# Performance work log

Measured on AMD Instinct MI355X. Metric: run time of the kernel, lower is better.

## Reference

```python
import jax, jax.numpy as jnp
import numpy as np

SR = 16000
N_FFT = 400
HOP = 160
N_MELS = 128
F_MIN = 0.0
F_MAX = 8000.0
PCEN_ALPHA = 0.8
PCEN_SMOOTH = 0.04
PCEN_DELTA = 2.0
PCEN_ROOT = 2.0
PCEN_FLOOR = 1e-08
TARGET = (192, 128)


def _hz_to_mel(f):
    return 2595.0 * np.log10(1.0 + f / 700.0)


def _mel_to_hz(m):
    return 700.0 * (10.0 ** (m / 2595.0) - 1.0)


def _mel_filterbank():
    # torchaudio melscale_fbanks, mel_scale='htk', norm=None
    n_freqs = N_FFT // 2 + 1  # 201
    all_freqs = np.linspace(0.0, SR / 2, n_freqs)
    m_pts = np.linspace(_hz_to_mel(F_MIN), _hz_to_mel(F_MAX), N_MELS + 2)
    f_pts = _mel_to_hz(m_pts)
    f_diff = f_pts[1:] - f_pts[:-1]  # (n_mels+1,)
    slopes = f_pts[None, :] - all_freqs[:, None]  # (n_freqs, n_mels+2)
    down = -slopes[:, :-2] / f_diff[:-1]
    up = slopes[:, 2:] / f_diff[1:]
    fb = np.maximum(0.0, np.minimum(down, up))  # (n_freqs, n_mels)
    return jnp.asarray(fb, dtype=jnp.float32)


def _hann_window():
    # periodic hann, matches torch.hann_window(400)
    n = np.arange(N_FFT)
    return jnp.asarray(0.5 * (1.0 - np.cos(2.0 * np.pi * n / N_FFT)), dtype=jnp.float32)


def setup_inputs() -> dict:
    key = jax.random.key(0)
    audio = jax.random.normal(key, (2048, 32000), dtype=jnp.float32)
    return {"audio": audio}


def _mel_spectrogram(audio):
    # center=True reflect pad by n_fft//2
    pad = N_FFT // 2
    x = jnp.pad(audio, ((0, 0), (pad, pad)), mode='reflect')  # (N, 32400)
    T = (x.shape[1] - N_FFT) // HOP + 1  # 201
    idx = jnp.arange(T)[:, None] * HOP + jnp.arange(N_FFT)[None, :]  # (T, n_fft)
    frames = x[:, idx] * _hann_window()  # (N, T, n_fft)
    spec = jnp.fft.rfft(frames, axis=-1)  # (N, T, 201)
    power = jnp.abs(spec) ** 2
    mel = jnp.einsum('ntf,fm->ntm', power, _mel_filterbank())  # (N, T, n_mels)
    return mel


def _pcen(mel_ntm):
    # IIR smoothing over time via scan; mel_ntm: (N, T, M)
    s = PCEN_SMOOTH
    mel_t = jnp.transpose(mel_ntm, (1, 0, 2))  # (T, N, M)

    def step(m_prev, e):
        m_new = (1.0 - s) * m_prev + s * e
        return m_new, m_new

    m0 = mel_t[0]
    _, Ms = jax.lax.scan(step, m0, mel_t[1:])
    M = jnp.concatenate([m0[None], Ms], axis=0)  # (T, N, Mels)
    M = jnp.transpose(M, (1, 0, 2))  # (N, T, Mels)
    inv_r = 1.0 / PCEN_ROOT
    return (mel_ntm / (PCEN_FLOOR + M) ** PCEN_ALPHA + PCEN_DELTA) ** inv_r - PCEN_DELTA ** inv_r


def reference(audio):
    mel = _mel_spectrogram(audio)          # (N, T, 128); original is (N,128,T), PCEN over time either way
    pcen = _pcen(mel)                      # (N, T, 128) == original after transpose(1,2)
    x = pcen[:, None, :, :]                # (N, 1, T, 128)
    N = x.shape[0]
    # bilinear, align_corners=False == jax.image 'linear' (half-pixel centers)
    out = jax.image.resize(x, (N, 1, TARGET[0], TARGET[1]), method='linear')
    return out
```

## Files before the change

kernel.cpp:

```cpp
#include <hip/hip_runtime.h>
#include <math.h>

typedef __attribute__((ext_vector_type(8))) _Float16 half8;
typedef __attribute__((ext_vector_type(4))) float f32x4;
typedef __attribute__((ext_vector_type(4))) unsigned int u32x4;

namespace {
constexpr int NS = 32000, PAD = 200, NT = 201, TOUT = 192, NMEL = 128;
constexpr int FRB = 48, NSTRIP = 5;
constexpr int AU_SPAN = 7936;
constexpr int PW_STRIDE = 232, PW_ROWS = 48;
constexpr int BAS_NT = 28;
constexpr int BAS_ELEMS = 13 * 28 * 64 * 8;
constexpr int FB_ELEMS  = 7 * 8 * 64 * 8;
constexpr int OUT_ROW_U16 = TOUT * NMEL * 2;
constexpr int MEL_OFF_U16 = OUT_ROW_U16 - NT * NMEL;
}

__device__ __forceinline__ int swz(int e) { return e ^ (((e >> 7) & 3) << 3); }
__device__ __forceinline__ unsigned short f2h(float f) {
  _Float16 h = (_Float16)f; return __builtin_bit_cast(unsigned short, h);
}
__device__ __forceinline__ float h2f(unsigned short u) {
  return (float)__builtin_bit_cast(_Float16, u);
}

__global__ void setup_tables(unsigned short* __restrict__ ws) {
  int idx = blockIdx.x * 256 + threadIdx.x;
  if (idx < BAS_ELEMS) {
    int j = idx & 7, lane = (idx >> 3) & 63, rest = idx >> 9;
    int nt = rest % BAS_NT, ks = rest / BAS_NT;
    int k   = ks * 32 + ((lane >> 4) << 3) + j;
    int col = nt * 16 + (lane & 15);
    float v = 0.f;
    if (k < 400 && col < 402) {
      int bin = col >> 1;
      int mm  = (k * bin) % 400;
      float th = (float)mm * 0.015707963267948967f;
      float tr = (col & 1) ? sinf(th) : cosf(th);
      float wn = 0.5f * (1.0f - cosf((float)k * 0.015707963267948967f));
      v = wn * tr;
    }
    ws[idx] = f2h(v);
  } else if (idx < BAS_ELEMS + FB_ELEMS) {
    int i2 = idx - BAS_ELEMS;
    int j = i2 & 7, lane = (i2 >> 3) & 63, rest = i2 >> 9;
    int nt = rest % 8, ks = rest / 8;
    int k   = ks * 32 + ((lane >> 4) << 3) + j;
    int mel = nt * 16 + (lane & 15);
    float v = 0.f;
    if (k <= 200) {
      double mhi = 2595.0 * log10(1.0 + 8000.0 / 700.0);
      double ml = mhi * (double)mel / 129.0;
      double mc = mhi * (double)(mel + 1) / 129.0;
      double mr = mhi * (double)(mel + 2) / 129.0;
      double fl = 700.0 * (pow(10.0, ml / 2595.0) - 1.0);
      double fc = 700.0 * (pow(10.0, mc / 2595.0) - 1.0);
      double fr = 700.0 * (pow(10.0, mr / 2595.0) - 1.0);
      double f  = 40.0 * (double)k;
      double wv = fmin((f - fl) / (fc - fl), (fr - f) / (fr - fc));
      v = (float)fmax(0.0, wv);
    }
    ws[idx] = f2h(v);
  }
}

__global__ __launch_bounds__(256) __attribute__((amdgpu_waves_per_eu(4)))
void dft_mel_kernel(const float* __restrict__ audio, const unsigned short* __restrict__ ws,
                    unsigned short* __restrict__ outu)
{
  __shared__ unsigned short au[AU_SPAN];
  __shared__ unsigned short pw16[PW_ROWS * PW_STRIDE];
  const int tid = threadIdx.x;
  const int bid = blockIdx.x;
  const int r = bid / NSTRIP, s = bid % NSTRIP;
  const int t0 = s * FRB;
  const float* __restrict__ ab = audio + (size_t)r * NS;
  const int g0 = t0 * 160 - PAD;

  {
    const int nchunk = AU_SPAN / 8;
    const int live   = (s == NSTRIP - 1) ? 224 : nchunk;
    #pragma unroll 4
    for (int ci = tid; ci < nchunk; ci += 256) {
      half8 hv;
      if (ci >= live) {
        hv = (half8){0, 0, 0, 0, 0, 0, 0, 0};
      } else {
        int gbase = g0 + ci * 8;
        if (gbase >= 0 && gbase + 7 < NS) {
          const float4* p = (const float4*)(ab + gbase);
          float4 x0 = p[0], x1 = p[1];
          hv[0] = (_Float16)x0.x; hv[1] = (_Float16)x0.y;
          hv[2] = (_Float16)x0.z; hv[3] = (_Float16)x0.w;
          hv[4] = (_Float16)x1.x; hv[5] = (_Float16)x1.y;
          hv[6] = (_Float16)x1.z; hv[7] = (_Float16)x1.w;
        } else {
          #pragma unroll
          for (int j = 0; j < 8; ++j) {
            int g = gbase + j;
            if (g < 0) g = -g;
            if (g >= NS) g = 2 * NS - 2 - g;
            hv[j] = (_Float16)ab[g];
          }
        }
      }
      *(half8*)(au + swz(ci * 8)) = hv;
    }
  }
  for (int i = tid; i < PW_ROWS * 32; i += 256) {
    int row = i >> 5, sl = i & 31;
    if (sl) pw16[row * PW_STRIDE + 200 + sl] = 0;
  }
  __syncthreads();

  const int w = tid >> 6, lane = tid & 63, lr = lane & 15, lg = lane >> 4;

  f32x4 acc[3][7];
  #pragma unroll
  for (int mm = 0; mm < 3; ++mm)
    #pragma unroll
    for (int n = 0; n < 7; ++n) acc[mm][n] = (f32x4){0.f, 0.f, 0.f, 0.f};
  {
    const int laneA = lr * 160 + lg * 8;
    for (int ks = 0; ks < 13; ++ks) {
      half8 Af[3];
      #pragma unroll
      for (int mm = 0; mm < 3; ++mm)
        Af[mm] = *(const half8*)(au + swz(mm * 2560 + ks * 32 + laneA));
      const unsigned short* bsrc = ws + ((size_t)((ks * BAS_NT + w * 7) * 64 + lane)) * 8;
      #pragma unroll
      for (int n = 0; n < 7; ++n) {
        half8 Bf = *(const half8*)(bsrc + n * 512);
        #pragma unroll
        for (int mm = 0; mm < 3; ++mm)
          acc[mm][n] = __builtin_amdgcn_mfma_f32_16x16x32_f16(Af[mm], Bf, acc[mm][n], 0, 0, 0);
      }
    }
  }

  #pragma unroll
  for (int mm = 0; mm < 3; ++mm) {
    #pragma unroll
    for (int n = 0; n < 7; ++n) {
      int gcol = (w * 7 + n) * 16 + lr;
      #pragma unroll
      for (int j = 0; j < 4; ++j) {
        float v = acc[mm][n][j];
        float q = __shfl_xor(v, 1);
        int row = mm * 16 + lg * 4 + j;
        if (!(gcol & 1) && gcol < 402)
          pw16[row * PW_STRIDE + (gcol >> 1)] = f2h(fmaf(v, v, q * q));
      }
    }
  }
  __syncthreads();

  #pragma unroll
  for (int mt = 0; mt < 3; ++mt) {
    #pragma unroll
    for (int nt = 0; nt < 2; ++nt) {
      f32x4 a2 = (f32x4){0.f, 0.f, 0.f, 0.f};
      const unsigned short* psrc = pw16 + (mt * 16 + lr) * PW_STRIDE + lg * 8;
      const unsigned short* fsrc = ws + BAS_ELEMS + ((size_t)(2 * w + nt) * 64 + lane) * 8;
      #pragma unroll
      for (int ks = 0; ks < 7; ++ks)
        a2 = __builtin_amdgcn_mfma_f32_16x16x32_f16(*(const half8*)(psrc + ks * 32),
                                                    *(const half8*)(fsrc + (size_t)ks * 4096),
                                                    a2, 0, 0, 0);
      int gm = (2 * w + nt) * 16 + lr;
      #pragma unroll
      for (int j = 0; j < 4; ++j) {
        int t = t0 + mt * 16 + lg * 4 + j;
        if (t < NT)
          outu[(size_t)r * OUT_ROW_U16 + MEL_OFF_U16 + t * NMEL + gm] = f2h(a2[j]);
      }
    }
  }
}

__global__ __launch_bounds__(512)
void pcen_resize_kernel(unsigned short* __restrict__ outu)
{
  __shared__ unsigned short mel[NT * NMEL];
  __shared__ float carry[4][NMEL];
  __shared__ float minb[4][NMEL];
  const int tid = threadIdx.x;
  const int r = blockIdx.x;
  const unsigned short* src = outu + (size_t)r * OUT_ROW_U16 + MEL_OFF_U16;
  for (int i = tid; i < (NT * NMEL) / 8; i += 512)
    *(u32x4*)(mel + i * 8) = *(const u32x4*)(src + (size_t)i * 8);
  __syncthreads();

  const int m = tid & 127, c = tid >> 7;
  const int t0  = (c == 0) ? 0 : (51 + 50 * (c - 1));
  const int len = (c == 0) ? 51 : 50;

  float M = 0.f;
  for (int t = t0; t < t0 + len; ++t) {
    float e = h2f(mel[t * NMEL + m]);
    M = (t == 0) ? e : fmaf(0.96f, M, 0.04f * e);
  }
  carry[c][m] = M;
  __syncthreads();
  if (c == 0) {
    float a50 = exp2f(50.0f * log2f(0.96f));
    float m1 = carry[0][m];
    float m2 = fmaf(a50, m1, carry[1][m]);
    float m3 = fmaf(a50, m2, carry[2][m]);
    minb[1][m] = m1; minb[2][m] = m2; minb[3][m] = m3;
  }
  __syncthreads();

  float Min = (c == 0) ? 0.f : minb[c][m];
  float wf = 1.f, Mloc = 0.f;
  for (int t = t0; t < t0 + len; ++t) {
    float e = h2f(mel[t * NMEL + m]);
    Mloc = (t == 0) ? e : fmaf(0.96f, Mloc, 0.04f * e);
    wf *= 0.96f;
    float Mt = fmaf(wf, Min, Mloc);
    float dn = exp2f(0.8f * log2f(1e-8f + Mt));
    float pc = sqrtf(e / dn + 2.0f) - 1.41421356237309515f;
    mel[t * NMEL + m] = f2h(pc);
  }
  __syncthreads();

  float* __restrict__ ob = (float*)outu + (size_t)r * TOUT * NMEL;
  const float INVS = 201.0f / 192.0f;
  for (int i = c; i < TOUT; i += 4) {
    float ct = ((float)i + 0.5f) * INVS - 0.5f;
    int jlo = (int)ceilf(ct - INVS);
    int jhi = (int)floorf(ct + INVS);
    if (jlo < 0) jlo = 0;
    if (jhi > NT - 1) jhi = NT - 1;
    float wsum = 0.f, val = 0.f;
    for (int j = jlo; j <= jhi; ++j) {
      float wv = 1.0f - fabsf((float)j - ct) / INVS;
      if (wv > 0.f) { wsum += wv; val = fmaf(wv, h2f(mel[j * NMEL + m]), val); }
    }
    ob[(size_t)i * NMEL + m] = val / wsum;
  }
}

extern "C" void kernel_launch(void* const* d_in, const int* in_sizes, int n_in,
                              void* d_out, int out_size, void* d_ws, size_t ws_size,
                              hipStream_t stream) {
  (void)in_sizes; (void)n_in; (void)out_size; (void)ws_size;
  unsigned short* ws = (unsigned short*)d_ws;
  setup_tables<<<(BAS_ELEMS + FB_ELEMS + 255) / 256, 256, 0, stream>>>(ws);
  dft_mel_kernel<<<2048 * NSTRIP, 256, 0, stream>>>((const float*)d_in[0], ws,
                                                    (unsigned short*)d_out);
  pcen_resize_kernel<<<2048, 512, 0, stream>>>((unsigned short*)d_out);
}
```

Before: 458.9 us.

## Split DFT-mel into full strips plus small tail kernel, prefetch basis

The old strip decomposition ran five 48-frame strips per row, and the last strip mostly computed zero-padded frames. The kernel is now templated: four full 48-frame strips per row, plus a separate single-tile launch for the remaining frames 192-200, so less padding work is done. The DFT loop now software-prefetches the next basis fragment. The shuffle is replaced by a DPP swap, and each lane writes its power values without a parity-conditional store. The filterbank fragments are hoisted into registers and reused across row tiles, and waves_per_eu is lowered to 3. An extra kernel launch and higher register pressure may offset some of this.

New measurement: 464.7 us. About the same (+1.3%).

```diff
diff --git a/kernel.cpp b/kernel.cpp
--- a/kernel.cpp
+++ b/kernel.cpp
@@ -7,9 +7,7 @@
 
 namespace {
 constexpr int NS = 32000, PAD = 200, NT = 201, TOUT = 192, NMEL = 128;
-constexpr int FRB = 48, NSTRIP = 5;
-constexpr int AU_SPAN = 7936;
-constexpr int PW_STRIDE = 232, PW_ROWS = 48;
+constexpr int PW_STRIDE = 236;
 constexpr int BAS_NT = 28;
 constexpr int BAS_ELEMS = 13 * 28 * 64 * 8;
 constexpr int FB_ELEMS  = 7 * 8 * 64 * 8;
@@ -65,115 +63,129 @@
   }
 }
 
-__global__ __launch_bounds__(256) __attribute__((amdgpu_waves_per_eu(4)))
+template <int MT>
+__global__ __launch_bounds__(256) __attribute__((amdgpu_waves_per_eu(3)))
 void dft_mel_kernel(const float* __restrict__ audio, const unsigned short* __restrict__ ws,
                     unsigned short* __restrict__ outu)
 {
-  __shared__ unsigned short au[AU_SPAN];
-  __shared__ unsigned short pw16[PW_ROWS * PW_STRIDE];
+  constexpr int AU = (MT == 3) ? 7936 : 2816;
+  __shared__ unsigned short au[AU];
+  __shared__ unsigned short pw16[MT * 16 * PW_STRIDE];
   const int tid = threadIdx.x;
   const int bid = blockIdx.x;
-  const int r = bid / NSTRIP, s = bid % NSTRIP;
-  const int t0 = s * FRB;
+  const int r  = (MT == 3) ? (bid >> 2) : bid;
+  const int t0 = (MT == 3) ? ((bid & 3) * 48) : 192;
   const float* __restrict__ ab = audio + (size_t)r * NS;
   const int g0 = t0 * 160 - PAD;
 
   {
-    const int nchunk = AU_SPAN / 8;
-    const int live   = (s == NSTRIP - 1) ? 224 : nchunk;
+    constexpr int nchunk = AU / 8;
     #pragma unroll 4
     for (int ci = tid; ci < nchunk; ci += 256) {
       half8 hv;
-      if (ci >= live) {
-        hv = (half8){0, 0, 0, 0, 0, 0, 0, 0};
+      int gbase = g0 + ci * 8;
+      if (gbase >= 0 && gbase + 7 < NS) {
+        const float4* p = (const float4*)(ab + gbase);
+        float4 x0 = p[0], x1 = p[1];
+        hv[0] = (_Float16)x0.x; hv[1] = (_Float16)x0.y;
+        hv[2] = (_Float16)x0.z; hv[3] = (_Float16)x0.w;
+        hv[4] = (_Float16)x1.x; hv[5] = (_Float16)x1.y;
+        hv[6] = (_Float16)x1.z; hv[7] = (_Float16)x1.w;
       } else {
-        int gbase = g0 + ci * 8;
-        if (gbase >= 0 && gbase + 7 < NS) {
-          const float4* p = (const float4*)(ab + gbase);
-          float4 x0 = p[0], x1 = p[1];
-          hv[0] = (_Float16)x0.x; hv[1] = (_Float16)x0.y;
-          hv[2] = (_Float16)x0.z; hv[3] = (_Float16)x0.w;
-          hv[4] = (_Float16)x1.x; hv[5] = (_Float16)x1.y;
-          hv[6] = (_Float16)x1.z; hv[7] = (_Float16)x1.w;
-        } else {
-          #pragma unroll
-          for (int j = 0; j < 8; ++j) {
-            int g = gbase + j;
-            if (g < 0) g = -g;
-            if (g >= NS) g = 2 * NS - 2 - g;
-            hv[j] = (_Float16)ab[g];
-          }
+        #pragma unroll
+        for (int j = 0; j < 8; ++j) {
+          int g = gbase + j;
+          if (g < 0) g = -g;
+          if (g >= NS) g = 2 * NS - 2 - g;
+          hv[j] = (_Float16)ab[g];
         }
       }
       *(half8*)(au + swz(ci * 8)) = hv;
     }
   }
-  for (int i = tid; i < PW_ROWS * 32; i += 256) {
-    int row = i >> 5, sl = i & 31;
-    if (sl) pw16[row * PW_STRIDE + 200 + sl] = 0;
-  }
   __syncthreads();
 
   const int w = tid >> 6, lane = tid & 63, lr = lane & 15, lg = lane >> 4;
 
-  f32x4 acc[3][7];
+  f32x4 acc[MT][7];
   #pragma unroll
-  for (int mm = 0; mm < 3; ++mm)
+  for (int mm = 0; mm < MT; ++mm)
     #pragma unroll
     for (int n = 0; n < 7; ++n) acc[mm][n] = (f32x4){0.f, 0.f, 0.f, 0.f};
   {
     const int laneA = lr * 160 + lg * 8;
+    const unsigned short* bptr = ws + ((size_t)(w * 7 * 64 + lane)) * 8;
+    half8 Bcur = *(const half8*)bptr;
     for (int ks = 0; ks < 13; ++ks) {
-      half8 Af[3];
-      #pragma unroll
-      for (int mm = 0; mm < 3; ++mm)
+      half8 Af[MT];
+      #pragma unroll
+      for (int mm = 0; mm < MT; ++mm)
         Af[mm] = *(const half8*)(au + swz(mm * 2560 + ks * 32 + laneA));
-      const unsigned short* bsrc = ws + ((size_t)((ks * BAS_NT + w * 7) * 64 + lane)) * 8;
       #pragma unroll
       for (int n = 0; n < 7; ++n) {
-        half8 Bf = *(const half8*)(bsrc + n * 512);
-        #pragma unroll
-        for (int mm = 0; mm < 3; ++mm)
-          acc[mm][n] = __builtin_amdgcn_mfma_f32_16x16x32_f16(Af[mm], Bf, acc[mm][n], 0, 0, 0);
-      }
-    }
-  }
+        half8 Bnext = Bcur;
+        if (n < 6)        Bnext = *(const half8*)(bptr + (n + 1) * 512);
+        else if (ks < 12) Bnext = *(const half8*)(bptr + BAS_NT * 512);
+        #pragma unroll
+        for (int mm = 0; mm < MT; ++mm)
+          acc[mm][n] = __builtin_amdgcn_mfma_f32_16x16x32_f16(Af[mm], Bcur, acc[mm][n], 0, 0, 0);
+        Bcur = Bnext;
+      }
+      bptr += BAS_NT * 512;
+    }
+  }
+  __syncthreads();
 
   #pragma unroll
-  for (int mm = 0; mm < 3; ++mm) {
+  for (int mm = 0; mm < MT; ++mm) {
     #pragma unroll
     for (int n = 0; n < 7; ++n) {
       int gcol = (w * 7 + n) * 16 + lr;
+      int bin  = gcol >> 1;
+      float p[4];
       #pragma unroll
       for (int j = 0; j < 4; ++j) {
         float v = acc[mm][n][j];
-        float q = __shfl_xor(v, 1);
-        int row = mm * 16 + lg * 4 + j;
-        if (!(gcol & 1) && gcol < 402)
-          pw16[row * PW_STRIDE + (gcol >> 1)] = f2h(fmaf(v, v, q * q));
-      }
-    }
-  }
-  __syncthreads();
-
-  #pragma unroll
-  for (int mt = 0; mt < 3; ++mt) {
-    #pragma unroll
-    for (int nt = 0; nt < 2; ++nt) {
-      f32x4 a2 = (f32x4){0.f, 0.f, 0.f, 0.f};
+        int iv = __builtin_bit_cast(int, v);
+        float q = __builtin_bit_cast(float,
+            __builtin_amdgcn_mov_dpp(iv, 0xB1, 0xF, 0xF, true));
+        p[j] = fmaf(v, v, q * q);
+      }
+      bool odd = (lr & 1);
+      int rowb = mm * 16 + lg * 4 + (odd ? 2 : 0);
+      pw16[rowb * PW_STRIDE + bin]       = f2h(odd ? p[2] : p[0]);
+      pw16[(rowb + 1) * PW_STRIDE + bin] = f2h(odd ? p[3] : p[1]);
+    }
+  }
+  __syncthreads();
+
+  {
+    half8 Fb[2][7];
+    const unsigned short* fbase = ws + BAS_ELEMS + (size_t)lane * 8;
+    #pragma unroll
+    for (int nt = 0; nt < 2; ++nt)
+      #pragma unroll
+      for (int ks = 0; ks < 7; ++ks)
+        Fb[nt][ks] = *(const half8*)(fbase + ((size_t)(ks * 8 + 2 * w + nt)) * 512);
+    #pragma unroll
+    for (int mt = 0; mt < MT; ++mt) {
+      half8 Pa[7];
       const unsigned short* psrc = pw16 + (mt * 16 + lr) * PW_STRIDE + lg * 8;
-      const unsigned short* fsrc = ws + BAS_ELEMS + ((size_t)(2 * w + nt) * 64 + lane) * 8;
-      #pragma unroll
-      for (int ks = 0; ks < 7; ++ks)
-        a2 = __builtin_amdgcn_mfma_f32_16x16x32_f16(*(const half8*)(psrc + ks * 32),
-                                                    *(const half8*)(fsrc + (size_t)ks * 4096),
-                                                    a2, 0, 0, 0);
-      int gm = (2 * w + nt) * 16 + lr;
-      #pragma unroll
-      for (int j = 0; j < 4; ++j) {
-        int t = t0 + mt * 16 + lg * 4 + j;
-        if (t < NT)
-          outu[(size_t)r * OUT_ROW_U16 + MEL_OFF_U16 + t * NMEL + gm] = f2h(a2[j]);
+      #pragma unroll
+      for (int ks = 0; ks < 7; ++ks) Pa[ks] = *(const half8*)(psrc + ks * 32);
+      #pragma unroll
+      for (int nt = 0; nt < 2; ++nt) {
+        f32x4 a2 = (f32x4){0.f, 0.f, 0.f, 0.f};
+        #pragma unroll
+        for (int ks = 0; ks < 7; ++ks)
+          a2 = __builtin_amdgcn_mfma_f32_16x16x32_f16(Pa[ks], Fb[nt][ks], a2, 0, 0, 0);
+        int gm = (2 * w + nt) * 16 + lr;
+        #pragma unroll
+        for (int j = 0; j < 4; ++j) {
+          int t = t0 + mt * 16 + lg * 4 + j;
+          if (MT == 3 || t < NT)
+            outu[(size_t)r * OUT_ROW_U16 + MEL_OFF_U16 + t * NMEL + gm] = f2h(a2[j]);
+        }
       }
     }
   }
@@ -248,7 +260,9 @@
   (void)in_sizes; (void)n_in; (void)out_size; (void)ws_size;
   unsigned short* ws = (unsigned short*)d_ws;
   setup_tables<<<(BAS_ELEMS + FB_ELEMS + 255) / 256, 256, 0, stream>>>(ws);
-  dft_mel_kernel<<<2048 * NSTRIP, 256, 0, stream>>>((const float*)d_in[0], ws,
-                                                    (unsigned short*)d_out);
+  dft_mel_kernel<3><<<2048 * 4, 256, 0, stream>>>((const float*)d_in[0], ws,
+                                                  (unsigned short*)d_out);
+  dft_mel_kernel<1><<<2048, 256, 0, stream>>>((const float*)d_in[0], ws,
+                                              (unsigned short*)d_out);
   pcen_resize_kernel<<<2048, 512, 0, stream>>>((unsigned short*)d_out);
 }
```
